# Kernel optimization log

Hardware: AMD Instinct MI355X
Metric: run time of the kernel (lower is better)

Reference implementation:

```python
import jax, jax.numpy as jnp
import numpy as np

NUM_LAYERS = 4
D_MODEL = 512
N_HEADS = 8
SEQ = 2048
HIDE = 2048


def setup_inputs() -> dict:
    key = jax.random.key(0)
    ks = jax.random.split(key, 18)
    L, D, Hd = NUM_LAYERS, D_MODEL, HIDE
    s = 0.02
    return {
        "x": jax.random.normal(ks[0], (2, SEQ, D), jnp.float32),
        "qw": jax.random.normal(ks[1], (L, D, D), jnp.float32) * s,
        "qb": jax.random.normal(ks[2], (L, D), jnp.float32) * s,
        "kw": jax.random.normal(ks[3], (L, D, D), jnp.float32) * s,
        "kb": jax.random.normal(ks[4], (L, D), jnp.float32) * s,
        "vw": jax.random.normal(ks[5], (L, D, D), jnp.float32) * s,
        "vb": jax.random.normal(ks[6], (L, D), jnp.float32) * s,
        "ow": jax.random.normal(ks[7], (L, D, D), jnp.float32) * s,
        "ob": jax.random.normal(ks[8], (L, D), jnp.float32) * s,
        "w0": jax.random.normal(ks[9], (L, D, Hd), jnp.float32) * s,
        "b0": jax.random.normal(ks[10], (L, Hd), jnp.float32) * s,
        "w1": jax.random.normal(ks[11], (L, D, Hd), jnp.float32) * s,
        "b1": jax.random.normal(ks[12], (L, Hd), jnp.float32) * s,
        "w2": jax.random.normal(ks[13], (L, Hd, D), jnp.float32) * s,
        "b2": jax.random.normal(ks[14], (L, D), jnp.float32) * s,
        "att_norm_w": jax.random.normal(ks[15], (L, D), jnp.float32),
        "ffn_norm_w": jax.random.normal(ks[16], (L, D), jnp.float32),
    }


def _rmsnorm(x, w):
    # w * x / (mean(x^2, -1)^0.5 + 1e-6)  -- eps added OUTSIDE the sqrt, as in source
    return w * x / (jnp.sqrt(jnp.mean(x * x, axis=-1, keepdims=True)) + 1e-6)


def _attention(x, wq, bq, wk, bk, wv, bv, wo, bo, causal):
    B, S, D = x.shape
    H = N_HEADS
    hd = D // H
    q = (x @ wq + bq).reshape(B, S, H, hd).transpose(0, 2, 1, 3)  # BHSd
    k = (x @ wk + bk).reshape(B, S, H, hd).transpose(0, 2, 1, 3)
    v = (x @ wv + bv).reshape(B, S, H, hd).transpose(0, 2, 1, 3)
    scores = jnp.einsum("bhqd,bhkd->bhqk", q, k) / jnp.sqrt(jnp.float32(hd))
    scores = jax.nn.softmax(scores + causal, axis=-1)  # BHSS
    o = jnp.einsum("bhqk,bhkd->bhqd", scores, v)
    o = o.transpose(0, 2, 1, 3).reshape(B, S, D)
    return o @ wo + bo


def reference(x, qw, qb, kw, kb, vw, vb, ow, ob, w0, b0, w1, b1, w2, b2, att_norm_w, ffn_norm_w):
    S = x.shape[1]
    # upper-triangular (excl. diag) additive -inf mask, as in the torch buffer
    causal = jnp.where(jnp.triu(jnp.ones((S, S), bool), k=1), -jnp.inf, 0.0).astype(x.dtype)
    h = x
    for i in range(NUM_LAYERS):
        a = _attention(_rmsnorm(h, att_norm_w[i]), qw[i], qb[i], kw[i], kb[i],
                       vw[i], vb[i], ow[i], ob[i], causal)
        h = a + h
        y = _rmsnorm(h, ffn_norm_w[i])
        y = ((y @ w0[i] + b0[i]) * jax.nn.silu(y @ w1[i] + b1[i])) @ w2[i] + b2[i]
        h = y + h
    return h
```

## Files before the change

kernel.cpp:

```cpp
#include <hip/hip_runtime.h>
#include <math.h>

typedef unsigned int   uint4v __attribute__((ext_vector_type(4)));
typedef float          f32x4  __attribute__((ext_vector_type(4)));
typedef __bf16         bf16x8 __attribute__((ext_vector_type(8)));
typedef unsigned short u16x8  __attribute__((ext_vector_type(8)));
typedef unsigned short u16x4  __attribute__((ext_vector_type(4)));

#define D_MODEL 512
#define SEQ     2048
#define BTOK    4096
#define HIDE    2048
#define NHEAD   8
#define HD      64

static __device__ __forceinline__ unsigned short f2bf(float f) {
  __bf16 b = (__bf16)f;
  return __builtin_bit_cast(unsigned short, b);
}
static __device__ __forceinline__ float bf2f(unsigned short b) {
  union { unsigned u; float f; } v; v.u = ((unsigned)b) << 16;
  return v.f;
}
static __device__ __forceinline__ bf16x8 ldb8(const unsigned short* p) {
  return __builtin_bit_cast(bf16x8, *(const uint4v*)p);
}
static __device__ __forceinline__ f32x4 mfma16(bf16x8 a, bf16x8 b, f32x4 c) {
  return __builtin_amdgcn_mfma_f32_16x16x32_bf16(a, b, c, 0, 0, 0);
}

typedef unsigned int u32_g __attribute__((address_space(1)));
typedef unsigned int u32_l __attribute__((address_space(3)));
static __device__ __forceinline__ void gload16(const unsigned short* g, unsigned short* l) {
  __builtin_amdgcn_global_load_lds((const u32_g*)(const void*)g,
                                   (u32_l*)(void*)l, 16, 0, 0);
}

#define SWZ(r, off) ((off) ^ (((r) & 7) << 4))
#define QSCALE 0.180336880f

template<int N>
static __device__ __forceinline__ void waitcnt_vm() {
  asm volatile("s_waitcnt vmcnt(%0)" :: "i"(N) : "memory");
}

__global__ __launch_bounds__(64) void prep_t(
    const float* __restrict__ qw, const float* __restrict__ kw,
    const float* __restrict__ vw, const float* __restrict__ ow,
    const float* __restrict__ w0, const float* __restrict__ w1,
    const float* __restrict__ w2,
    unsigned short* __restrict__ Wq, unsigned short* __restrict__ Wo,
    unsigned short* __restrict__ W01, unsigned short* __restrict__ W2)
{
  int bid = blockIdx.x;
  int l = bid >> 10;
  int r = bid & 1023;
  const float* src; unsigned short* dst;
  int tr, tc, srcN, dstK;
  if (r < 192) {
    int sel = r >> 6, tt = r & 63;
    tr = tt >> 3; tc = tt & 7;
    src = (sel == 0 ? qw : sel == 1 ? kw : vw) + (size_t)l * 262144;
    srcN = 512; dstK = 512;
    dst = Wq + (size_t)l * 786432 + (size_t)(sel * 512 + tc * 64) * 512 + tr * 64;
  } else if (r < 256) {
    int tt = r - 192; tr = tt >> 3; tc = tt & 7;
    src = ow + (size_t)l * 262144; srcN = 512; dstK = 512;
    dst = Wo + (size_t)l * 262144 + (size_t)(tc * 64) * 512 + tr * 64;
  } else if (r < 768) {
    int idx = r - 256; int sel = idx >> 8; int tt = idx & 255;
    tr = tt >> 5; tc = tt & 31;
    src = (sel ? w1 : w0) + (size_t)l * 1048576; srcN = 2048; dstK = 512;
    dst = W01 + (size_t)l * 2097152 + (size_t)sel * 1048576 + (size_t)(tc * 64) * 512 + tr * 64;
  } else {
    int tt = r - 768; tr = tt >> 3; tc = tt & 7;
    src = w2 + (size_t)l * 1048576; srcN = 512; dstK = 2048;
    dst = W2 + (size_t)l * 1048576 + (size_t)(tc * 64) * 2048 + tr * 64;
  }
  src += (size_t)(tr * 64) * srcN + tc * 64;
  __shared__ unsigned short T[64][68];
  int t = threadIdx.x;
  #pragma unroll
  for (int it = 0; it < 16; ++it) {
    int row = it * 4 + (t >> 4);
    int col = (t & 15) * 4;
    f32x4 v4 = *(const f32x4*)(src + (size_t)row * srcN + col);
    u16x4 o; o[0] = f2bf(v4.x); o[1] = f2bf(v4.y); o[2] = f2bf(v4.z); o[3] = f2bf(v4.w);
    *(u16x4*)&T[row][col] = o;
  }
  __syncthreads();
  unsigned short* orow = dst + (size_t)t * dstK;
  #pragma unroll
  for (int j0 = 0; j0 < 8; ++j0) {
    u16x8 o;
    #pragma unroll
    for (int j = 0; j < 8; ++j) o[j] = T[j0 * 8 + j][t];
    *(u16x8*)(orow + j0 * 8) = o;
  }
}

__global__ __launch_bounds__(256) void initrms_k(const float* __restrict__ x,
                                                 const float* __restrict__ w,
                                                 float* __restrict__ h,
                                                 unsigned short* __restrict__ xn) {
  int row  = blockIdx.x * 4 + (threadIdx.x >> 6);
  int lane = threadIdx.x & 63;
  const float* xr = x + (size_t)row * D_MODEL + lane * 8;
  f32x4 v0 = *(const f32x4*)(xr);
  f32x4 v1 = *(const f32x4*)(xr + 4);
  *(f32x4*)(h + (size_t)row * D_MODEL + lane * 8)     = v0;
  *(f32x4*)(h + (size_t)row * D_MODEL + lane * 8 + 4) = v1;
  float ss = v0.x*v0.x + v0.y*v0.y + v0.z*v0.z + v0.w*v0.w
           + v1.x*v1.x + v1.y*v1.y + v1.z*v1.z + v1.w*v1.w;
  #pragma unroll
  for (int m = 1; m < 64; m <<= 1) ss += __shfl_xor(ss, m, 64);
  float inv = 1.0f / (sqrtf(ss * (1.0f / D_MODEL)) + 1e-6f);
  f32x4 w0 = *(const f32x4*)(w + lane * 8);
  f32x4 w1 = *(const f32x4*)(w + lane * 8 + 4);
  u16x8 o;
  o[0] = f2bf(v0.x * w0.x * inv); o[1] = f2bf(v0.y * w0.y * inv);
  o[2] = f2bf(v0.z * w0.z * inv); o[3] = f2bf(v0.w * w0.w * inv);
  o[4] = f2bf(v1.x * w1.x * inv); o[5] = f2bf(v1.y * w1.y * inv);
  o[6] = f2bf(v1.z * w1.z * inv); o[7] = f2bf(v1.w * w1.w * inv);
  *(u16x8*)(xn + (size_t)row * D_MODEL + lane * 8) = o;
}

__global__ __launch_bounds__(256) void addrms_k(float* __restrict__ h,
                                                const unsigned short* __restrict__ y,
                                                const float* __restrict__ w,
                                                unsigned short* __restrict__ xn) {
  int row  = blockIdx.x * 4 + (threadIdx.x >> 6);
  int lane = threadIdx.x & 63;
  float* hr = h + (size_t)row * D_MODEL + lane * 8;
  f32x4 v0 = *(const f32x4*)(hr);
  f32x4 v1 = *(const f32x4*)(hr + 4);
  u16x8 yy = *(const u16x8*)(y + (size_t)row * D_MODEL + lane * 8);
  v0.x += bf2f(yy[0]); v0.y += bf2f(yy[1]); v0.z += bf2f(yy[2]); v0.w += bf2f(yy[3]);
  v1.x += bf2f(yy[4]); v1.y += bf2f(yy[5]); v1.z += bf2f(yy[6]); v1.w += bf2f(yy[7]);
  *(f32x4*)(hr)     = v0;
  *(f32x4*)(hr + 4) = v1;
  float ss = v0.x*v0.x + v0.y*v0.y + v0.z*v0.z + v0.w*v0.w
           + v1.x*v1.x + v1.y*v1.y + v1.z*v1.z + v1.w*v1.w;
  #pragma unroll
  for (int m = 1; m < 64; m <<= 1) ss += __shfl_xor(ss, m, 64);
  float inv = 1.0f / (sqrtf(ss * (1.0f / D_MODEL)) + 1e-6f);
  f32x4 w0 = *(const f32x4*)(w + lane * 8);
  f32x4 w1 = *(const f32x4*)(w + lane * 8 + 4);
  u16x8 o;
  o[0] = f2bf(v0.x * w0.x * inv); o[1] = f2bf(v0.y * w0.y * inv);
  o[2] = f2bf(v0.z * w0.z * inv); o[3] = f2bf(v0.w * w0.w * inv);
  o[4] = f2bf(v1.x * w1.x * inv); o[5] = f2bf(v1.y * w1.y * inv);
  o[6] = f2bf(v1.z * w1.z * inv); o[7] = f2bf(v1.w * w1.w * inv);
  *(u16x8*)(xn + (size_t)row * D_MODEL + lane * 8) = o;
}

#define EPI_QKV   0
#define EPI_PLAIN 1

template<int EPI, int BM, int BN>
__global__ __launch_bounds__(256) void gemm7_k(
    const unsigned short* __restrict__ A,
    const unsigned short* __restrict__ Bt,
    const float* __restrict__ bias0,
    const float* __restrict__ bias1,
    const float* __restrict__ bias2,
    void* __restrict__ out0,
    void* __restrict__ out1,
    void* __restrict__ out2,
    int M, int N, int K)
{
  constexpr int MF = BM / 32;
  constexpr int NF = BN / 32;
  constexpr int ALOADS = BM / 32;
  constexpr int BLOADS = BN / 32;
  constexpr int NL = ALOADS + BLOADS;

  __shared__ __attribute__((aligned(16))) unsigned short Al[2][BM * 64];
  __shared__ __attribute__((aligned(16))) unsigned short Bl[2][BN * 64];

  int nblk = gridDim.x;
  int orig = blockIdx.x;
  int qq = nblk >> 3, rr = nblk & 7, xcd = orig & 7, pos = orig >> 3;
  int lid = (xcd < rr ? xcd * (qq + 1) : rr * (qq + 1) + (xcd - rr) * qq) + pos;
  int numN = N / BN;
  int mt = lid / numN, nt = lid % numN;
  int m0 = mt * BM, n0 = nt * BN;

  int tid = threadIdx.x, lane = tid & 63, w = tid >> 6;
  int wm = w >> 1, wn = w & 1;
  int g = lane >> 4, c = lane & 15;
  int srow = lane >> 3, sslot = lane & 7;
  int sgc = (sslot ^ srow) * 8;

  const unsigned short* aG = A  + (size_t)(m0 + w * (BM / 4) + srow) * K + sgc;
  const unsigned short* bG = Bt + (size_t)(n0 + w * (BN / 4) + srow) * K + sgc;
  int aOff = (w * (BM / 4) + srow) * 64 + sslot * 8;
  int bOff = (w * (BN / 4) + srow) * 64 + sslot * 8;

  f32x4 acc[MF][NF] = {};
  int KT = K >> 6;
  int rk = c & 7;

  #pragma unroll
  for (int t = 0; t < ALOADS; ++t)
    gload16(aG + (size_t)(t * 8) * K, &Al[0][aOff + t * 8 * 64]);
  #pragma unroll
  for (int t = 0; t < BLOADS; ++t)
    gload16(bG + (size_t)(t * 8) * K, &Bl[0][bOff + t * 8 * 64]);

  for (int kt = 0; kt < KT; ++kt) {
    int cur = kt & 1;
    if (kt + 1 < KT) {
      int nb = cur ^ 1;
      const unsigned short* aGk = aG + (kt + 1) * 64;
      const unsigned short* bGk = bG + (kt + 1) * 64;
      #pragma unroll
      for (int t = 0; t < ALOADS; ++t)
        gload16(aGk + (size_t)(t * 8) * K, &Al[nb][aOff + t * 8 * 64]);
      #pragma unroll
      for (int t = 0; t < BLOADS; ++t)
        gload16(bGk + (size_t)(t * 8) * K, &Bl[nb][bOff + t * 8 * 64]);
      waitcnt_vm<NL>();
    } else {
      waitcnt_vm<0>();
    }
    __builtin_amdgcn_s_barrier();
    __builtin_amdgcn_sched_barrier(0);
    #pragma unroll
    for (int ks = 0; ks < 2; ++ks) {
      int slot = (ks * 4 + g) ^ rk;
      bf16x8 af[MF], bfr[NF];
      #pragma unroll
      for (int i = 0; i < MF; ++i)
        af[i] = ldb8(&Al[cur][(wm * (MF * 16) + i * 16 + c) * 64 + slot * 8]);
      #pragma unroll
      for (int j = 0; j < NF; ++j)
        bfr[j] = ldb8(&Bl[cur][(wn * (NF * 16) + j * 16 + c) * 64 + slot * 8]);
      #pragma unroll
      for (int i = 0; i < MF; ++i)
        #pragma unroll
        for (int j = 0; j < NF; ++j)
          acc[i][j] = mfma16(af[i], bfr[j], acc[i][j]);
    }
    __builtin_amdgcn_sched_barrier(0);
    __builtin_amdgcn_s_barrier();
  }

  if (EPI == EPI_QKV) {
    int sel  = n0 >> 9;
    if (sel < 2) {
      #pragma unroll
      for (int i = 0; i < MF; ++i) {
        int mrow = m0 + wm * (MF * 16) + i * 16 + g * 4;
        #pragma unroll
        for (int j = 0; j < NF; ++j) {
          int nloc = (n0 & 511) + wn * (NF * 16) + j * 16 + c;
          const float* bp = sel == 0 ? bias0 : bias1;
          unsigned short* o = (unsigned short*)(sel == 0 ? out0 : out1);
          float sc = (sel == 0) ? QSCALE : 1.0f;
          float bn = bp[nloc];
          #pragma unroll
          for (int ii = 0; ii < 4; ++ii)
            o[(size_t)(mrow + ii) * D_MODEL + nloc] = f2bf((acc[i][j][ii] + bn) * sc);
        }
      }
    } else {
      unsigned short* T = &Al[0][0];
      #pragma unroll
      for (int i = 0; i < MF; ++i) {
        int ml0 = wm * (MF * 16) + i * 16 + g * 4;
        #pragma unroll
        for (int j = 0; j < NF; ++j) {
          int nl = wn * (NF * 16) + j * 16 + c;
          float bn = bias2[(n0 & 511) + nl];
          u16x4 pk;
          #pragma unroll
          for (int ii = 0; ii < 4; ++ii) pk[ii] = f2bf(acc[i][j][ii] + bn);
          *(u16x4*)&T[nl * 136 + ml0] = pk;
        }
      }
      __syncthreads();
      int b  = m0 >> 11, s0 = m0 & 2047;
      int hh = (n0 & 511) >> 6;
      int r  = tid >> 2, c0 = (tid & 3) * 32;
      unsigned short* dst = (unsigned short*)out2 +
          ((size_t)(b * NHEAD + hh) * HD + r) * SEQ + s0 + c0;
      #pragma unroll
      for (int u = 0; u < 4; ++u)
        *(u16x8*)(dst + u * 8) = *(u16x8*)&T[r * 136 + c0 + u * 8];
    }
  } else {
    #pragma unroll
    for (int i = 0; i < MF; ++i) {
      int mrow = m0 + wm * (MF * 16) + i * 16 + g * 4;
      #pragma unroll
      for (int j = 0; j < NF; ++j) {
        int n = n0 + wn * (NF * 16) + j * 16 + c;
        float bn = bias0[n];
        unsigned short* o = (unsigned short*)out0;
        #pragma unroll
        for (int ii = 0; ii < 4; ++ii)
          o[(size_t)(mrow + ii) * N + n] = f2bf(acc[i][j][ii] + bn);
      }
    }
  }
}

template<int BM, int BN>
__global__ __launch_bounds__(256) void gemm7d_k(
    const unsigned short* __restrict__ A,
    const unsigned short* __restrict__ B0t,
    const unsigned short* __restrict__ B1t,
    const float* __restrict__ bias0,
    const float* __restrict__ bias1,
    unsigned short* __restrict__ out,
    int M, int N, int K)
{
  constexpr int MF = BM / 32;
  constexpr int NF = BN / 32;
  constexpr int ALOADS = BM / 32;
  constexpr int BLOADS = BN / 32;
  constexpr int NL = ALOADS + 2 * BLOADS;

  __shared__ __attribute__((aligned(16))) unsigned short Al[2][BM * 64];
  __shared__ __attribute__((aligned(16))) unsigned short B0l[2][BN * 64];
  __shared__ __attribute__((aligned(16))) unsigned short B1l[2][BN * 64];

  int nblk = gridDim.x;
  int orig = blockIdx.x;
  int qq = nblk >> 3, rr = nblk & 7, xcd = orig & 7, pos = orig >> 3;
  int lid = (xcd < rr ? xcd * (qq + 1) : rr * (qq + 1) + (xcd - rr) * qq) + pos;
  int numM = M / BM;
  int nt = lid / numM, mt = lid % numM;
  int m0 = mt * BM, n0 = nt * BN;

  int tid = threadIdx.x, lane = tid & 63, w = tid >> 6;
  int wm = w >> 1, wn = w & 1;
  int g = lane >> 4, c = lane & 15;
  int srow = lane >> 3, sslot = lane & 7;
  int sgc = (sslot ^ srow) * 8;

  const unsigned short* aG  = A   + (size_t)(m0 + w * (BM / 4) + srow) * K + sgc;
  const unsigned short* b0G = B0t + (size_t)(n0 + w * (BN / 4) + srow) * K + sgc;
  const unsigned short* b1G = B1t + (size_t)(n0 + w * (BN / 4) + srow) * K + sgc;
  int aOff = (w * (BM / 4) + srow) * 64 + sslot * 8;
  int bOff = (w * (BN / 4) + srow) * 64 + sslot * 8;

  f32x4 acc0[MF][NF] = {};
  f32x4 acc1[MF][NF] = {};
  int KT = K >> 6;
  int rk = c & 7;

  #pragma unroll
  for (int t = 0; t < ALOADS; ++t)
    gload16(aG + (size_t)(t * 8) * K, &Al[0][aOff + t * 8 * 64]);
  #pragma unroll
  for (int t = 0; t < BLOADS; ++t) {
    gload16(b0G + (size_t)(t * 8) * K, &B0l[0][bOff + t * 8 * 64]);
    gload16(b1G + (size_t)(t * 8) * K, &B1l[0][bOff + t * 8 * 64]);
  }

  for (int kt = 0; kt < KT; ++kt) {
    int cur = kt & 1;
    if (kt + 1 < KT) {
      int nb = cur ^ 1;
      const unsigned short* aGk  = aG  + (kt + 1) * 64;
      const unsigned short* b0Gk = b0G + (kt + 1) * 64;
      const unsigned short* b1Gk = b1G + (kt + 1) * 64;
      #pragma unroll
      for (int t = 0; t < ALOADS; ++t)
        gload16(aGk + (size_t)(t * 8) * K, &Al[nb][aOff + t * 8 * 64]);
      #pragma unroll
      for (int t = 0; t < BLOADS; ++t) {
        gload16(b0Gk + (size_t)(t * 8) * K, &B0l[nb][bOff + t * 8 * 64]);
        gload16(b1Gk + (size_t)(t * 8) * K, &B1l[nb][bOff + t * 8 * 64]);
      }
      waitcnt_vm<NL>();
    } else {
      waitcnt_vm<0>();
    }
    __builtin_amdgcn_s_barrier();
    __builtin_amdgcn_sched_barrier(0);
    #pragma unroll
    for (int ks = 0; ks < 2; ++ks) {
      int slot = (ks * 4 + g) ^ rk;
      bf16x8 af[MF], b0f[NF], b1f[NF];
      #pragma unroll
      for (int i = 0; i < MF; ++i)
        af[i] = ldb8(&Al[cur][(wm * (MF * 16) + i * 16 + c) * 64 + slot * 8]);
      #pragma unroll
      for (int j = 0; j < NF; ++j) {
        b0f[j] = ldb8(&B0l[cur][(wn * (NF * 16) + j * 16 + c) * 64 + slot * 8]);
        b1f[j] = ldb8(&B1l[cur][(wn * (NF * 16) + j * 16 + c) * 64 + slot * 8]);
      }
      #pragma unroll
      for (int i = 0; i < MF; ++i)
        #pragma unroll
        for (int j = 0; j < NF; ++j) {
          acc0[i][j] = mfma16(af[i], b0f[j], acc0[i][j]);
          acc1[i][j] = mfma16(af[i], b1f[j], acc1[i][j]);
        }
    }
    __builtin_amdgcn_sched_barrier(0);
    __builtin_amdgcn_s_barrier();
  }

  #pragma unroll
  for (int i = 0; i < MF; ++i) {
    int mrow = m0 + wm * (MF * 16) + i * 16 + g * 4;
    #pragma unroll
    for (int j = 0; j < NF; ++j) {
      int n = n0 + wn * (NF * 16) + j * 16 + c;
      float b0n = bias0[n], b1n = bias1[n];
      #pragma unroll
      for (int ii = 0; ii < 4; ++ii) {
        float a  = acc0[i][j][ii] + b0n;
        float gv = acc1[i][j][ii] + b1n;
        float s  = gv / (1.0f + __expf(-gv));
        out[(size_t)(mrow + ii) * N + n] = f2bf(a * s);
      }
    }
  }
}

struct Stg { uint4v k0, k1, v0, v1; };

static __device__ __forceinline__ Stg stage_load(const unsigned short* Kp,
                                                 const unsigned short* Vp,
                                                 int kbase, int srow, int sslot) {
  Stg s;
  const unsigned short* kr = Kp + (size_t)(kbase + srow) * D_MODEL + sslot * 8;
  s.k0 = *(const uint4v*)kr;
  s.k1 = *(const uint4v*)(kr + 32);
  const unsigned short* vr = Vp + (size_t)srow * SEQ + kbase + sslot * 8;
  s.v0 = *(const uint4v*)vr;
  s.v1 = *(const uint4v*)(vr + 32);
  return s;
}
static __device__ __forceinline__ void stage_write(unsigned short* Klb, unsigned short* Vlb,
                                                   const Stg& s, int srow, int sslot) {
  char* kb = (char*)Klb;
  *(uint4v*)(kb + SWZ(srow, srow * 128 + sslot * 16))       = s.k0;
  *(uint4v*)(kb + SWZ(srow, srow * 128 + (sslot + 4) * 16)) = s.k1;
  char* vb = (char*)Vlb;
  *(uint4v*)(vb + SWZ(srow, srow * 128 + sslot * 16))       = s.v0;
  *(uint4v*)(vb + SWZ(srow, srow * 128 + (sslot + 4) * 16)) = s.v1;
}

template<bool MASKED>
static __device__ __forceinline__ void attn_tile(
    const unsigned short* Klb, const unsigned short* Vlb,
    bf16x8 qf0, bf16x8 qf1, f32x4* oacc, float& ps,
    int g, int c, int kbase, int qrow)
{
  f32x4 z[4];
  #pragma unroll
  for (int hh = 0; hh < 4; ++hh) {
    int r = hh * 16 + c;
    const char* base = (const char*)Klb;
    bf16x8 k0 = ldb8((const unsigned short*)(base + SWZ(r, r * 128 + g * 16)));
    bf16x8 k1 = ldb8((const unsigned short*)(base + SWZ(r, r * 128 + 64 + g * 16)));
    f32x4 t = {};
    t = mfma16(k0, qf0, t);
    t = mfma16(k1, qf1, t);
    z[hh] = t;
  }
  u16x8 pa0, pa1;
  #pragma unroll
  for (int hh = 0; hh < 4; ++hh) {
    #pragma unroll
    for (int i = 0; i < 4; ++i) {
      float p = exp2f(z[hh][i]);
      if (MASKED && (kbase + hh * 16 + g * 4 + i > qrow)) p = 0.0f;
      ps += p;
      unsigned short pb = f2bf(p);
      if (hh < 2) pa0[hh * 4 + i] = pb;
      else        pa1[(hh - 2) * 4 + i] = pb;
    }
  }
  bf16x8 af0 = __builtin_bit_cast(bf16x8, pa0);
  bf16x8 af1 = __builtin_bit_cast(bf16x8, pa1);
  #pragma unroll
  for (int db = 0; db < 4; ++db) {
    int r = db * 16 + c;
    const char* base = (const char*)Vlb;
    u16x4 v00 = *(const u16x4*)(base + SWZ(r, r * 128 + g * 8));
    u16x4 v01 = *(const u16x4*)(base + SWZ(r, r * 128 + 32 + g * 8));
    u16x4 v10 = *(const u16x4*)(base + SWZ(r, r * 128 + 64 + g * 8));
    u16x4 v11 = *(const u16x4*)(base + SWZ(r, r * 128 + 96 + g * 8));
    u16x8 vb0, vb1;
    #pragma unroll
    for (int j = 0; j < 4; ++j) {
      vb0[j] = v00[j]; vb0[4 + j] = v01[j];
      vb1[j] = v10[j]; vb1[4 + j] = v11[j];
    }
    oacc[db] = mfma16(af0, __builtin_bit_cast(bf16x8, vb0), oacc[db]);
    oacc[db] = mfma16(af1, __builtin_bit_cast(bf16x8, vb1), oacc[db]);
  }
}

static __device__ __forceinline__ int slot_base(int c) {
  if (c < 16) return (c - 8) * 2;
  if (c < 24) return 16 + (c - 16) * 3;
  return 40 + (c - 24) * 4;
}

__global__ __launch_bounds__(256) void attn5_k(const unsigned short* __restrict__ Q,
                                               const unsigned short* __restrict__ K,
                                               const unsigned short* __restrict__ VT,
                                               unsigned short* __restrict__ O,
                                               float* __restrict__ Oparts,
                                               float* __restrict__ Sparts)
{
  __shared__ __attribute__((aligned(16))) unsigned short Kl[2][64 * 64];
  __shared__ __attribute__((aligned(16))) unsigned short Vl[2][64 * 64];
  int tid = threadIdx.x, lane = tid & 63, w = tid >> 6;
  int g = lane >> 4, cl = lane & 15;

  int z = 79 - (int)blockIdx.x;
  int c, sp;
  if (z < 8)        { c = z;                    sp = 0; }
  else if (z < 24)  { int t2 = z - 8;  c = 8  + (t2 >> 1); sp = t2 & 1; }
  else if (z < 48)  { int t2 = z - 24; c = 16 + t2 / 3;    sp = t2 % 3; }
  else              { int t2 = z - 48; c = 24 + (t2 >> 2); sp = t2 & 3; }
  int kt0 = sp * 8;
  int kt1 = min(c + 1, kt0 + 8);
  bool lastsplit = (kt1 == c + 1);

  int bh = blockIdx.y, b = bh >> 3, h = bh & 7;
  int q0 = c * 64;
  const unsigned short* Qp = Q + (size_t)(b * SEQ) * D_MODEL + h * HD;
  const unsigned short* Kp = K + (size_t)(b * SEQ) * D_MODEL + h * HD;
  const unsigned short* Vp = VT + (size_t)bh * HD * SEQ;

  int qrow = q0 + w * 16 + cl;
  bf16x8 qf0 = ldb8(Qp + (size_t)qrow * D_MODEL + g * 8);
  bf16x8 qf1 = ldb8(Qp + (size_t)qrow * D_MODEL + 32 + g * 8);

  f32x4 oacc[4] = {};
  float ps = 0.0f;
  int srow = tid >> 2, sslot = tid & 3;

  Stg s0 = stage_load(Kp, Vp, kt0 * 64, srow, sslot);
  stage_write(&Kl[0][0], &Vl[0][0], s0, srow, sslot);
  __syncthreads();

  int buf = 0;
  for (int kt = kt0; kt < kt1 - 1; ++kt) {
    Stg sn = stage_load(Kp, Vp, (kt + 1) * 64, srow, sslot);
    attn_tile<false>(&Kl[buf][0], &Vl[buf][0], qf0, qf1, oacc, ps, g, cl, 0, 0);
    stage_write(&Kl[buf ^ 1][0], &Vl[buf ^ 1][0], sn, srow, sslot);
    __syncthreads();
    buf ^= 1;
  }
  if (lastsplit)
    attn_tile<true>(&Kl[buf][0], &Vl[buf][0], qf0, qf1, oacc, ps, g, cl,
                    (kt1 - 1) * 64, qrow);
  else
    attn_tile<false>(&Kl[buf][0], &Vl[buf][0], qf0, qf1, oacc, ps, g, cl, 0, 0);

  ps += __shfl_xor(ps, 16, 64);
  ps += __shfl_xor(ps, 32, 64);

  if (c < 8) {
    f32x4 inv;
    #pragma unroll
    for (int i = 0; i < 4; ++i) inv[i] = 1.0f / __shfl(ps, g * 4 + i, 64);
    #pragma unroll
    for (int db = 0; db < 4; ++db)
      #pragma unroll
      for (int i = 0; i < 4; ++i)
        O[(size_t)(b * SEQ + q0 + w * 16 + g * 4 + i) * D_MODEL + h * HD + db * 16 + cl] =
            f2bf(oacc[db][i] * inv[i]);
  } else {
    size_t slot = (size_t)bh * 72 + slot_base(c) + sp;
    float* Op = Oparts + slot * 4096;
    float* Sp = Sparts + slot * 64;
    #pragma unroll
    for (int db = 0; db < 4; ++db)
      #pragma unroll
      for (int i = 0; i < 4; ++i)
        Op[(w * 16 + g * 4 + i) * 64 + db * 16 + cl] = oacc[db][i];
    if (g == 0) Sp[w * 16 + cl] = ps;
  }
}

__global__ __launch_bounds__(256) void attn_comb_k(const float* __restrict__ Oparts,
                                                   const float* __restrict__ Sparts,
                                                   unsigned short* __restrict__ O) {
  int t  = threadIdx.x;
  int c  = 8 + (int)(blockIdx.x % 24);
  int bh = (int)(blockIdx.x / 24);
  int b = bh >> 3, h = bh & 7;
  int ns = (c + 8) >> 3;
  size_t slot = (size_t)bh * 72 + slot_base(c);
  const float* O0 = Oparts + slot * 4096;
  const float* S0 = Sparts + slot * 64;
  int r = t >> 2, d0 = (t & 3) * 16;
  f32x4 a0 = {}, a1 = {}, a2 = {}, a3 = {};
  float s = 0.0f;
  for (int si = 0; si < ns; ++si) {
    const float* o = O0 + si * 4096 + r * 64 + d0;
    a0 += *(const f32x4*)(o);
    a1 += *(const f32x4*)(o + 4);
    a2 += *(const f32x4*)(o + 8);
    a3 += *(const f32x4*)(o + 12);
    s  += S0[si * 64 + r];
  }
  float inv = 1.0f / s;
  u16x8 w0, w1;
  #pragma unroll
  for (int j = 0; j < 4; ++j) {
    w0[j]     = f2bf(a0[j] * inv); w0[4 + j] = f2bf(a1[j] * inv);
    w1[j]     = f2bf(a2[j] * inv); w1[4 + j] = f2bf(a3[j] * inv);
  }
  unsigned short* dst = O + (size_t)(b * SEQ + c * 64 + r) * D_MODEL + h * HD + d0;
  *(u16x8*)(dst)     = w0;
  *(u16x8*)(dst + 8) = w1;
}

extern "C" void kernel_launch(void* const* d_in, const int* in_sizes, int n_in,
                              void* d_out, int out_size, void* d_ws, size_t ws_size,
                              hipStream_t stream) {
  (void)in_sizes; (void)n_in; (void)out_size; (void)ws_size;
  const float* x   = (const float*)d_in[0];
  const float* qw  = (const float*)d_in[1];
  const float* qb  = (const float*)d_in[2];
  const float* kw  = (const float*)d_in[3];
  const float* kbi = (const float*)d_in[4];
  const float* vw  = (const float*)d_in[5];
  const float* vb  = (const float*)d_in[6];
  const float* ow  = (const float*)d_in[7];
  const float* ob  = (const float*)d_in[8];
  const float* w0  = (const float*)d_in[9];
  const float* b0  = (const float*)d_in[10];
  const float* w1  = (const float*)d_in[11];
  const float* b1  = (const float*)d_in[12];
  const float* w2  = (const float*)d_in[13];
  const float* b2  = (const float*)d_in[14];
  const float* anw = (const float*)d_in[15];
  const float* fnw = (const float*)d_in[16];

  char* ws = (char*)d_ws;
  float*          h    = (float*)ws;
  unsigned short* xn   = (unsigned short*)(ws + (8u  << 20));
  unsigned short* q    = (unsigned short*)(ws + (12u << 20));
  unsigned short* k    = (unsigned short*)(ws + (16u << 20));
  unsigned short* vt   = (unsigned short*)(ws + (24u << 20));
  unsigned short* ao   = (unsigned short*)(ws + (28u << 20));
  unsigned short* y    = (unsigned short*)(ws + (32u << 20));
  unsigned short* hbuf = (unsigned short*)(ws + (12u << 20));
  unsigned short* Wq   = (unsigned short*)(ws + (36u << 20));
  unsigned short* Wo   = (unsigned short*)(ws + (42u << 20));
  unsigned short* W01  = (unsigned short*)(ws + (44u << 20));
  unsigned short* W2   = (unsigned short*)(ws + (60u << 20));
  float*          Opar = (float*)(ws + (68u << 20));
  float*          Spar = (float*)(ws + (86u << 20));

  prep_t<<<4096, 64, 0, stream>>>(qw, kw, vw, ow, w0, w1, w2, Wq, Wo, W01, W2);
  initrms_k<<<BTOK / 4, 256, 0, stream>>>(x, anw, h, xn);

  for (int l = 0; l < 4; ++l) {
    size_t bo  = (size_t)l * D_MODEL;
    size_t bho = (size_t)l * HIDE;

    gemm7_k<EPI_QKV, 128, 64><<<768, 256, 0, stream>>>(
        xn, Wq + (size_t)l * 786432, qb + bo, kbi + bo, vb + bo,
        q, k, vt, BTOK, 3 * D_MODEL, D_MODEL);
    attn5_k<<<dim3(80, 16), 256, 0, stream>>>(q, k, vt, ao, Opar, Spar);
    attn_comb_k<<<384, 256, 0, stream>>>(Opar, Spar, ao);
    gemm7_k<EPI_PLAIN, 64, 64><<<512, 256, 0, stream>>>(
        ao, Wo + (size_t)l * 262144, ob + bo, nullptr, nullptr,
        y, nullptr, nullptr, BTOK, D_MODEL, D_MODEL);
    addrms_k<<<BTOK / 4, 256, 0, stream>>>(h, y, fnw + bo, xn);

    gemm7d_k<128, 64><<<1024, 256, 0, stream>>>(
        xn, W01 + (size_t)l * 2097152, W01 + (size_t)l * 2097152 + 1048576,
        b0 + bho, b1 + bho, hbuf, BTOK, HIDE, D_MODEL);
    gemm7_k<EPI_PLAIN, 64, 64><<<512, 256, 0, stream>>>(
        hbuf, W2 + (size_t)l * 1048576, b2 + bo, nullptr, nullptr,
        y, nullptr, nullptr, BTOK, D_MODEL, HIDE);
    addrms_k<<<BTOK / 4, 256, 0, stream>>>(
        h, y, (l < 3 ? anw + bo + D_MODEL : anw), xn);
  }
  hipMemcpyAsync(d_out, h, (size_t)BTOK * D_MODEL * sizeof(float),
                 hipMemcpyDeviceToDevice, stream);
}
```

Measured before the change: 467.4 us.

## Single-buffer dual FFN GEMM, enlarge W2 tile, write final residual directly

The gate/up FFN GEMM drops double-buffered LDS prefetch in favour of a single buffer with syncthreads around each k-step. This halves LDS use, which may raise occupancy, but it loses the overlap of loads with compute. The down-projection GEMM moves to 128x64 tiles with half the blocks. The last layer's residual add writes straight into the output, replacing the extra RMSNorm pass and the device-to-device copy.

```diff
diff --git a/kernel.cpp b/kernel.cpp
--- a/kernel.cpp
+++ b/kernel.cpp
@@ -154,6 +154,21 @@
   *(u16x8*)(xn + (size_t)row * D_MODEL + lane * 8) = o;
 }
 
+__global__ __launch_bounds__(256) void addout_k(const float* __restrict__ h,
+                                                const unsigned short* __restrict__ y,
+                                                float* __restrict__ out) {
+  int row  = blockIdx.x * 4 + (threadIdx.x >> 6);
+  int lane = threadIdx.x & 63;
+  const float* hr = h + (size_t)row * D_MODEL + lane * 8;
+  f32x4 v0 = *(const f32x4*)(hr);
+  f32x4 v1 = *(const f32x4*)(hr + 4);
+  u16x8 yy = *(const u16x8*)(y + (size_t)row * D_MODEL + lane * 8);
+  v0.x += bf2f(yy[0]); v0.y += bf2f(yy[1]); v0.z += bf2f(yy[2]); v0.w += bf2f(yy[3]);
+  v1.x += bf2f(yy[4]); v1.y += bf2f(yy[5]); v1.z += bf2f(yy[6]); v1.w += bf2f(yy[7]);
+  *(f32x4*)(out + (size_t)row * D_MODEL + lane * 8)     = v0;
+  *(f32x4*)(out + (size_t)row * D_MODEL + lane * 8 + 4) = v1;
+}
+
 #define EPI_QKV   0
 #define EPI_PLAIN 1
 
@@ -307,7 +322,7 @@
 }
 
 template<int BM, int BN>
-__global__ __launch_bounds__(256) void gemm7d_k(
+__global__ __launch_bounds__(256) void gemm10d_k(
     const unsigned short* __restrict__ A,
     const unsigned short* __restrict__ B0t,
     const unsigned short* __restrict__ B1t,
@@ -320,11 +335,10 @@
   constexpr int NF = BN / 32;
   constexpr int ALOADS = BM / 32;
   constexpr int BLOADS = BN / 32;
-  constexpr int NL = ALOADS + 2 * BLOADS;
-
-  __shared__ __attribute__((aligned(16))) unsigned short Al[2][BM * 64];
-  __shared__ __attribute__((aligned(16))) unsigned short B0l[2][BN * 64];
-  __shared__ __attribute__((aligned(16))) unsigned short B1l[2][BN * 64];
+
+  __shared__ __attribute__((aligned(16))) unsigned short Al[BM * 64];
+  __shared__ __attribute__((aligned(16))) unsigned short B0l[BN * 64];
+  __shared__ __attribute__((aligned(16))) unsigned short B1l[BN * 64];
 
   int nblk = gridDim.x;
   int orig = blockIdx.x;
@@ -343,55 +357,37 @@
   const unsigned short* aG  = A   + (size_t)(m0 + w * (BM / 4) + srow) * K + sgc;
   const unsigned short* b0G = B0t + (size_t)(n0 + w * (BN / 4) + srow) * K + sgc;
   const unsigned short* b1G = B1t + (size_t)(n0 + w * (BN / 4) + srow) * K + sgc;
-  int aOff = (w * (BM / 4) + srow) * 64 + sslot * 8;
-  int bOff = (w * (BN / 4) + srow) * 64 + sslot * 8;
+  unsigned short* aL  = &Al [(w * (BM / 4) + srow) * 64 + sslot * 8];
+  unsigned short* b0L = &B0l[(w * (BN / 4) + srow) * 64 + sslot * 8];
+  unsigned short* b1L = &B1l[(w * (BN / 4) + srow) * 64 + sslot * 8];
 
   f32x4 acc0[MF][NF] = {};
   f32x4 acc1[MF][NF] = {};
   int KT = K >> 6;
   int rk = c & 7;
 
-  #pragma unroll
-  for (int t = 0; t < ALOADS; ++t)
-    gload16(aG + (size_t)(t * 8) * K, &Al[0][aOff + t * 8 * 64]);
-  #pragma unroll
-  for (int t = 0; t < BLOADS; ++t) {
-    gload16(b0G + (size_t)(t * 8) * K, &B0l[0][bOff + t * 8 * 64]);
-    gload16(b1G + (size_t)(t * 8) * K, &B1l[0][bOff + t * 8 * 64]);
-  }
-
   for (int kt = 0; kt < KT; ++kt) {
-    int cur = kt & 1;
-    if (kt + 1 < KT) {
-      int nb = cur ^ 1;
-      const unsigned short* aGk  = aG  + (kt + 1) * 64;
-      const unsigned short* b0Gk = b0G + (kt + 1) * 64;
-      const unsigned short* b1Gk = b1G + (kt + 1) * 64;
-      #pragma unroll
-      for (int t = 0; t < ALOADS; ++t)
-        gload16(aGk + (size_t)(t * 8) * K, &Al[nb][aOff + t * 8 * 64]);
-      #pragma unroll
-      for (int t = 0; t < BLOADS; ++t) {
-        gload16(b0Gk + (size_t)(t * 8) * K, &B0l[nb][bOff + t * 8 * 64]);
-        gload16(b1Gk + (size_t)(t * 8) * K, &B1l[nb][bOff + t * 8 * 64]);
-      }
-      waitcnt_vm<NL>();
-    } else {
-      waitcnt_vm<0>();
-    }
-    __builtin_amdgcn_s_barrier();
-    __builtin_amdgcn_sched_barrier(0);
+    if (kt) __syncthreads();
+    #pragma unroll
+    for (int t = 0; t < ALOADS; ++t)
+      gload16(aG + (size_t)(t * 8) * K + kt * 64, aL + t * 8 * 64);
+    #pragma unroll
+    for (int t = 0; t < BLOADS; ++t) {
+      gload16(b0G + (size_t)(t * 8) * K + kt * 64, b0L + t * 8 * 64);
+      gload16(b1G + (size_t)(t * 8) * K + kt * 64, b1L + t * 8 * 64);
+    }
+    __syncthreads();
     #pragma unroll
     for (int ks = 0; ks < 2; ++ks) {
       int slot = (ks * 4 + g) ^ rk;
       bf16x8 af[MF], b0f[NF], b1f[NF];
       #pragma unroll
       for (int i = 0; i < MF; ++i)
-        af[i] = ldb8(&Al[cur][(wm * (MF * 16) + i * 16 + c) * 64 + slot * 8]);
+        af[i] = ldb8(&Al[(wm * (MF * 16) + i * 16 + c) * 64 + slot * 8]);
       #pragma unroll
       for (int j = 0; j < NF; ++j) {
-        b0f[j] = ldb8(&B0l[cur][(wn * (NF * 16) + j * 16 + c) * 64 + slot * 8]);
-        b1f[j] = ldb8(&B1l[cur][(wn * (NF * 16) + j * 16 + c) * 64 + slot * 8]);
+        b0f[j] = ldb8(&B0l[(wn * (NF * 16) + j * 16 + c) * 64 + slot * 8]);
+        b1f[j] = ldb8(&B1l[(wn * (NF * 16) + j * 16 + c) * 64 + slot * 8]);
       }
       #pragma unroll
       for (int i = 0; i < MF; ++i)
@@ -401,8 +397,6 @@
           acc1[i][j] = mfma16(af[i], b1f[j], acc1[i][j]);
         }
     }
-    __builtin_amdgcn_sched_barrier(0);
-    __builtin_amdgcn_s_barrier();
   }
 
   #pragma unroll
@@ -674,15 +668,15 @@
         y, nullptr, nullptr, BTOK, D_MODEL, D_MODEL);
     addrms_k<<<BTOK / 4, 256, 0, stream>>>(h, y, fnw + bo, xn);
 
-    gemm7d_k<128, 64><<<1024, 256, 0, stream>>>(
+    gemm10d_k<128, 64><<<1024, 256, 0, stream>>>(
         xn, W01 + (size_t)l * 2097152, W01 + (size_t)l * 2097152 + 1048576,
         b0 + bho, b1 + bho, hbuf, BTOK, HIDE, D_MODEL);
-    gemm7_k<EPI_PLAIN, 64, 64><<<512, 256, 0, stream>>>(
+    gemm7_k<EPI_PLAIN, 128, 64><<<256, 256, 0, stream>>>(
         hbuf, W2 + (size_t)l * 1048576, b2 + bo, nullptr, nullptr,
         y, nullptr, nullptr, BTOK, D_MODEL, HIDE);
-    addrms_k<<<BTOK / 4, 256, 0, stream>>>(
-        h, y, (l < 3 ? anw + bo + D_MODEL : anw), xn);
-  }
-  hipMemcpyAsync(d_out, h, (size_t)BTOK * D_MODEL * sizeof(float),
-                 hipMemcpyDeviceToDevice, stream);
-}
+    if (l < 3)
+      addrms_k<<<BTOK / 4, 256, 0, stream>>>(h, y, anw + bo + D_MODEL, xn);
+    else
+      addout_k<<<BTOK / 4, 256, 0, stream>>>(h, y, (float*)d_out);
+  }
+}
```

New measurement: 483.4 us. 1.03x slower.
